# Kernel optimization log

Measured on AMD Instinct MI355X. Metric: run time of the kernel, lower is better.

## Reference

```python
import jax, jax.numpy as jnp
import numpy as np

NUM_HEADS = 8
EPS = 1e-12  # tf.nn.l2_normalize epsilon


def _l2_normalize(t):
    # tf.nn.l2_normalize: x * rsqrt(max(sum(x^2), eps)) along last axis
    sq = jnp.sum(t * t, axis=-1, keepdims=True)
    return t * jax.lax.rsqrt(jnp.maximum(sq, EPS))


def setup_inputs() -> dict:
    key = jax.random.key(0)
    ks = jax.random.split(key, 4)
    B, N, C = 8, 4096, 512
    x = jax.random.normal(ks[0], (B, N, C), dtype=jnp.float32)
    w_qkv = jax.random.normal(ks[1], (C, 3 * C), dtype=jnp.float32) * (C ** -0.5)
    b_qkv = jnp.zeros((3 * C,), dtype=jnp.float32)
    w_proj = jax.random.normal(ks[2], (C, C), dtype=jnp.float32) * (C ** -0.5)
    b_proj = jnp.zeros((C,), dtype=jnp.float32)
    return {"x": x, "w_qkv": w_qkv, "b_qkv": b_qkv, "w_proj": w_proj, "b_proj": b_proj}


def reference(x, w_qkv, b_qkv, w_proj, b_proj):
    B, N, C = x.shape
    h = NUM_HEADS
    d = C // h
    scale = d ** -0.5
    qkv = x @ w_qkv + b_qkv                        # [B,N,3C]
    qkv = qkv.reshape(B, N, 3, h, d)
    qkv = jnp.transpose(qkv, (2, 0, 3, 1, 4))      # [3,B,h,N,d]
    q, k, v = qkv[0], qkv[1], qkv[2]
    q = _l2_normalize(q) * scale
    k = _l2_normalize(k)
    # channel-wise attention: q^T k over tokens -> [B,h,d,d]
    attn = jnp.einsum('bhnd,bhne->bhde', q, k)
    attn = jax.nn.softmax(attn, axis=-1)
    out = jnp.einsum('bhnd,bhde->bhne', v, attn)   # [B,h,N,d]
    out = jnp.transpose(out, (0, 2, 1, 3)).reshape(B, N, C)
    out = out @ w_proj + b_proj
    return out
```

## Files before the change

kernel.cpp:

```cpp
#include <hip/hip_runtime.h>
#include <stdint.h>

#define NB 8
#define NN 4096
#define NC 512
#define NH 8
#define ATTN_CH 16

typedef __bf16 bf16x8 __attribute__((ext_vector_type(8)));
typedef float floatx4 __attribute__((ext_vector_type(4)));

__device__ __forceinline__ unsigned short f2bf(float f) {
  union { float f; unsigned u; } v; v.f = f;
  return (unsigned short)((v.u + 0x7fffu + ((v.u >> 16) & 1u)) >> 16);
}
__device__ __forceinline__ float2 bfp2f(unsigned u) {
  union { unsigned x; float f; } lo, hi;
  lo.x = u << 16; hi.x = u & 0xffff0000u;
  return make_float2(lo.f, hi.f);
}

__device__ __forceinline__ void async_ld16(void* lds, const void* g) {
  auto* gp = (const __attribute__((address_space(1))) unsigned int*)(uintptr_t)g;
  auto* lp = (__attribute__((address_space(3))) unsigned int*)(uintptr_t)lds;
  __builtin_amdgcn_global_load_lds(gp, lp, 16, 0, 0);
}

__global__ __launch_bounds__(256) void k_prep(const float* __restrict__ x,
                                              unsigned short* __restrict__ xb,
                                              const float* __restrict__ w,
                                              unsigned short* __restrict__ wt) {
  int bid = blockIdx.x;
  if (bid < 16384) {
    int i = (bid * 256 + threadIdx.x) * 4;
    float4 v = *(const float4*)(x + i);
    ushort4 o;
    o.x = f2bf(v.x); o.y = f2bf(v.y); o.z = f2bf(v.z); o.w = f2bf(v.w);
    *(ushort4*)(xb + i) = o;
    return;
  }
  __shared__ float tile[64][65];
  int b2 = bid - 16384;
  int nn0 = (b2 % 24) * 64, kk0 = (b2 / 24) * 64;
  int t = threadIdx.x;
#pragma unroll
  for (int i = 0; i < 16; i++) {
    int id = t + i * 256;
    int r = id >> 6, c = id & 63;
    tile[c][r] = w[(size_t)(kk0 + r) * 1536 + nn0 + c];
  }
  __syncthreads();
#pragma unroll
  for (int i = 0; i < 16; i++) {
    int id = t + i * 256;
    int rn = id >> 6, ck = id & 63;
    wt[(size_t)(nn0 + rn) * 512 + kk0 + ck] = f2bf(tile[rn][ck]);
  }
}

__global__ __launch_bounds__(256, 2) void k_gemm_qkv(const unsigned short* __restrict__ A,
                                                     const unsigned short* __restrict__ Bt,
                                                     const float* __restrict__ bias,
                                                     unsigned short* __restrict__ Cq) {
  const int LDA = 512, LDB = 512, LDC = 1536;
  int bid = blockIdx.x;
  int xcd = bid & 7, local = bid >> 3;
  int mloc = local / 12, nt = local - mloc * 12;
  int m0 = (xcd * 32 + mloc) * 128, n0 = nt * 128;

  int tid = threadIdx.x;
  int lane = tid & 63, w = tid >> 6;
  int wm = (w & 1) * 64, wn = (w >> 1) * 64;
  int quad = lane >> 4, rr = lane & 15;
  int r8 = lane >> 3, cg = lane & 7;
  int cgs8 = (cg ^ r8) * 8;
  const int swz = rr & 7;

  __shared__ __align__(16) unsigned short Als[3][128 * 64];
  __shared__ __align__(16) unsigned short Bls[2][128 * 64];

  floatx4 acc[4][4];
#pragma unroll
  for (int i = 0; i < 4; i++)
#pragma unroll
    for (int j = 0; j < 4; j++) acc[i][j] = (floatx4){0.f, 0.f, 0.f, 0.f};

  auto stageA = [&](int ss, int kt) {
    int k0 = kt << 6;
#pragma unroll
    for (int i = 0; i < 4; i++) {
      int rb = i * 32 + w * 8;
      async_ld16(&Als[ss][rb * 64], A + (size_t)(m0 + rb + r8) * LDA + k0 + cgs8);
    }
  };
  auto stageB = [&](int ss, int kt) {
    int k0 = kt << 6;
#pragma unroll
    for (int i = 0; i < 4; i++) {
      int rb = i * 32 + w * 8;
      async_ld16(&Bls[ss][rb * 64], Bt + (size_t)(n0 + rb + r8) * LDB + k0 + cgs8);
    }
  };

  auto computeK = [&](int sa, int sb, int gb) {
    bf16x8 af[4], bfr[4];
#pragma unroll
    for (int mi = 0; mi < 4; mi++)
      af[mi] = *(const bf16x8*)&Als[sa][(wm + mi * 16 + rr) * 64 + (((gb + quad) ^ swz)) * 8];
#pragma unroll
    for (int ni = 0; ni < 4; ni++)
      bfr[ni] = *(const bf16x8*)&Bls[sb][(wn + ni * 16 + rr) * 64 + (((gb + quad) ^ swz)) * 8];
    __builtin_amdgcn_s_setprio(1);
#pragma unroll
    for (int mi = 0; mi < 4; mi++)
#pragma unroll
      for (int ni = 0; ni < 4; ni++)
        acc[mi][ni] = __builtin_amdgcn_mfma_f32_16x16x32_bf16(af[mi], bfr[ni], acc[mi][ni], 0, 0, 0);
    __builtin_amdgcn_s_setprio(0);
  };

  stageB(0, 0); stageA(0, 0); stageA(1, 1);
  int sa = 0;
#pragma unroll 1
  for (int t = 0; t < 8; t++) {
    if (t < 7) asm volatile("s_waitcnt vmcnt(4)" ::: "memory");
    else       asm volatile("s_waitcnt vmcnt(0)" ::: "memory");
    asm volatile("s_barrier" ::: "memory");
    if (t < 7) stageB((t + 1) & 1, t + 1);
    if (t < 6) { int s2 = sa + 2; if (s2 >= 3) s2 -= 3; stageA(s2, t + 2); }
    __builtin_amdgcn_sched_barrier(0);
    computeK(sa, t & 1, 0);
    computeK(sa, t & 1, 4);
    sa = (sa + 1 < 3) ? sa + 1 : 0;
  }

#pragma unroll
  for (int ni = 0; ni < 4; ni++) {
    int col = n0 + wn + ni * 16 + rr;
    float bv = bias[col];
#pragma unroll
    for (int mi = 0; mi < 4; mi++) {
      int rbase = m0 + wm + mi * 16 + quad * 4;
#pragma unroll
      for (int r = 0; r < 4; r++)
        Cq[(size_t)(rbase + r) * LDC + col] = f2bf(acc[mi][ni][r] + bv);
    }
  }
}

__global__ __launch_bounds__(256) void k_attn(const unsigned short* __restrict__ QKV,
                                              float* __restrict__ logits_p) {
  int chunk = blockIdx.x, hh = blockIdx.y, b = blockIdx.z;
  int tid = threadIdx.x, w = tid >> 6, l = tid & 63;
  int quad = l >> 4, rr = l & 15;

  __shared__ __align__(16) unsigned char smem[40960];
  unsigned short* qT = (unsigned short*)smem + w * 5120;
  unsigned short* kT = qT + 2560;
  float* ps = (float*)smem;

  floatx4 acc[4][4];
#pragma unroll
  for (int i = 0; i < 4; i++)
#pragma unroll
    for (int j = 0; j < 4; j++) acc[i][j] = (floatx4){0.f, 0.f, 0.f, 0.f};

  int tok8 = l >> 3;
  int seg = l & 7;
  int sw = seg & 3;

  for (int s = 0; s < 2; s++) {
    int nbase = chunk * 256 + w * 64 + s * 32;
#pragma unroll
    for (int c = 0; c < 4; c++) {
      int n = nbase + c * 8 + tok8;
      const unsigned short* p = QKV + (size_t)(b * 4096 + n) * 1536 + hh * 64 + seg * 8;
      uint4 vq = *(const uint4*)p;
      uint4 vk = *(const uint4*)(p + 512);
      unsigned uq[4] = {vq.x, vq.y, vq.z, vq.w};
      unsigned uk[4] = {vk.x, vk.y, vk.z, vk.w};
      float qf[8], kf[8], sq = 0.f, sk = 0.f;
#pragma unroll
      for (int e = 0; e < 4; e++) {
        float2 f = bfp2f(uq[e]); qf[2 * e] = f.x; qf[2 * e + 1] = f.y; sq += f.x * f.x + f.y * f.y;
        float2 g = bfp2f(uk[e]); kf[2 * e] = g.x; kf[2 * e + 1] = g.y; sk += g.x * g.x + g.y * g.y;
      }
      sq += __shfl_xor(sq, 1); sq += __shfl_xor(sq, 2); sq += __shfl_xor(sq, 4);
      sk += __shfl_xor(sk, 1); sk += __shfl_xor(sk, 2); sk += __shfl_xor(sk, 4);
      float scq = 0.125f * rsqrtf(fmaxf(sq, 1e-12f));
      float sck = rsqrtf(fmaxf(sk, 1e-12f));
      int col = ((c ^ sw) << 3) + tok8;
#pragma unroll
      for (int j = 0; j < 8; j++) {
        int dim = seg * 8 + j;
        qT[dim * 40 + col] = f2bf(qf[j] * scq);
        kT[dim * 40 + col] = f2bf(kf[j] * sck);
      }
    }
    bf16x8 af[4], bfr[4];
#pragma unroll
    for (int mi = 0; mi < 4; mi++) {
      int s3 = (mi * 2 + (rr >> 3)) & 3;
      int off = (mi * 16 + rr) * 40 + ((quad ^ s3) << 3);
      af[mi] = *(const bf16x8*)(qT + off);
      bfr[mi] = *(const bf16x8*)(kT + off);
    }
#pragma unroll
    for (int mi = 0; mi < 4; mi++)
#pragma unroll
      for (int ni = 0; ni < 4; ni++)
        acc[mi][ni] = __builtin_amdgcn_mfma_f32_16x16x32_bf16(af[mi], bfr[ni], acc[mi][ni], 0, 0, 0);
  }

  __syncthreads();
  for (int r2 = 0; r2 < 4; r2++) {
    if (w == r2) {
#pragma unroll
      for (int mi = 0; mi < 4; mi++)
#pragma unroll
        for (int ni = 0; ni < 4; ni++)
#pragma unroll
          for (int r = 0; r < 4; r++) {
            int d = mi * 16 + quad * 4 + r, e = ni * 16 + rr;
            if (r2 == 0) ps[d * 64 + e] = acc[mi][ni][r];
            else         ps[d * 64 + e] += acc[mi][ni][r];
          }
    }
    __syncthreads();
  }
  float* outp = logits_p + ((size_t)(b * 8 + hh) * ATTN_CH + chunk) * 4096;
  for (int i = tid; i < 4096; i += 256) outp[i] = ps[i];
}

__global__ __launch_bounds__(256) void k_softmax_m(const float* __restrict__ logits_p,
                                                   const float* __restrict__ wproj,
                                                   unsigned short* __restrict__ Mt) {
  int cc = blockIdx.x & 3, rh = blockIdx.x >> 2;
  int hh = blockIdx.y, b = blockIdx.z;
  int t = threadIdx.x;
  __shared__ float ls[32][64];
  __shared__ float red[32][8];
  __shared__ float inv[32];
  const float* lp = logits_p + (size_t)((b * 8 + hh) * ATTN_CH) * 4096 + rh * 2048;
#pragma unroll
  for (int i = 0; i < 8; i++) {
    int id = t + i * 256;
    float s = 0.f;
#pragma unroll
    for (int c = 0; c < ATTN_CH; c++) s += lp[c * 4096 + id];
    ls[id >> 6][id & 63] = s;
  }
  __syncthreads();
  int row = t >> 3, part = t & 7;
  float mx = -1e30f;
#pragma unroll
  for (int j = 0; j < 8; j++) mx = fmaxf(mx, ls[row][part * 8 + j]);
  red[row][part] = mx;
  __syncthreads();
  if (part == 0) {
    float m2 = red[row][0];
#pragma unroll
    for (int j = 1; j < 8; j++) m2 = fmaxf(m2, red[row][j]);
    inv[row] = m2;
  }
  __syncthreads();
  float rm = inv[row];
  float s = 0.f;
#pragma unroll
  for (int j = 0; j < 8; j++) {
    float e = __expf(ls[row][part * 8 + j] - rm);
    ls[row][part * 8 + j] = e;
    s += e;
  }
  red[row][part] = s;
  __syncthreads();
  if (part == 0) {
    float s2 = 0.f;
#pragma unroll
    for (int j = 0; j < 8; j++) s2 += red[row][j];
    inv[row] = 1.0f / s2;
  }
  __syncthreads();

  int cout = cc * 128 + (t & 127);
  int half = t >> 7;
  float wreg[64];
#pragma unroll
  for (int ee = 0; ee < 64; ee++) wreg[ee] = wproj[(size_t)(hh * 64 + ee) * 512 + cout];
  unsigned short ob[16];
#pragma unroll
  for (int d2 = 0; d2 < 16; d2++) {
    int dd = half * 16 + d2;
    float a = 0.f;
#pragma unroll
    for (int e4 = 0; e4 < 16; e4++) {
      float4 p4 = *(const float4*)&ls[dd][e4 * 4];
      a += p4.x * wreg[e4 * 4] + p4.y * wreg[e4 * 4 + 1] + p4.z * wreg[e4 * 4 + 2] + p4.w * wreg[e4 * 4 + 3];
    }
    ob[d2] = f2bf(a * inv[dd]);
  }
  uint4* dst = (uint4*)(Mt + ((size_t)(b * 512 + cout)) * 512 + hh * 64 + rh * 32 + half * 16);
  dst[0] = ((const uint4*)ob)[0];
  dst[1] = ((const uint4*)ob)[1];
}

__global__ __launch_bounds__(256, 2) void k_gemm_out(const unsigned short* __restrict__ QKV,
                                                     const unsigned short* __restrict__ MtAll,
                                                     const float* __restrict__ bias,
                                                     float* __restrict__ Out) {
  const int LDA = 1536, LDB = 512, LDC = 512;
  int bid = blockIdx.x;
  int xcd = bid & 7, local = bid >> 3;
  int mloc = local >> 2, nt = local & 3;
  int g = xcd * 32 + mloc;
  int b = g >> 5;
  int m0 = (g & 31) * 128;
  int n0 = nt * 128;
  const unsigned short* A = QKV + (size_t)b * NN * 1536 + 1024;
  const unsigned short* Bt = MtAll + (size_t)b * 512 * 512;
  int tid = threadIdx.x;
  int lane = tid & 63, w = tid >> 6;
  int wm = (w & 1) * 64, wn = (w >> 1) * 64;
  int quad = lane >> 4, rr = lane & 15;
  int r8 = lane >> 3, cg = lane & 7;
  int cgs8 = (cg ^ r8) * 8;
  const int swz = rr & 7;

  __shared__ __align__(16) unsigned short Als[3][128 * 64];
  __shared__ __align__(16) unsigned short Bls[2][128 * 64];

  floatx4 acc[4][4];
#pragma unroll
  for (int i = 0; i < 4; i++)
#pragma unroll
    for (int j = 0; j < 4; j++) acc[i][j] = (floatx4){0.f, 0.f, 0.f, 0.f};

  auto stageA = [&](int ss, int kt) {
    int k0 = kt << 6;
#pragma unroll
    for (int i = 0; i < 4; i++) {
      int rb = i * 32 + w * 8;
      async_ld16(&Als[ss][rb * 64], A + (size_t)(m0 + rb + r8) * LDA + k0 + cgs8);
    }
  };
  auto stageB = [&](int ss, int kt) {
    int k0 = kt << 6;
#pragma unroll
    for (int i = 0; i < 4; i++) {
      int rb = i * 32 + w * 8;
      async_ld16(&Bls[ss][rb * 64], Bt + (size_t)(n0 + rb + r8) * LDB + k0 + cgs8);
    }
  };

  auto computeK = [&](int sa, int sb, int gb) {
    bf16x8 af[4], bfr[4];
#pragma unroll
    for (int mi = 0; mi < 4; mi++)
      af[mi] = *(const bf16x8*)&Als[sa][(wm + mi * 16 + rr) * 64 + (((gb + quad) ^ swz)) * 8];
#pragma unroll
    for (int ni = 0; ni < 4; ni++)
      bfr[ni] = *(const bf16x8*)&Bls[sb][(wn + ni * 16 + rr) * 64 + (((gb + quad) ^ swz)) * 8];
    __builtin_amdgcn_s_setprio(1);
#pragma unroll
    for (int mi = 0; mi < 4; mi++)
#pragma unroll
      for (int ni = 0; ni < 4; ni++)
        acc[mi][ni] = __builtin_amdgcn_mfma_f32_16x16x32_bf16(af[mi], bfr[ni], acc[mi][ni], 0, 0, 0);
    __builtin_amdgcn_s_setprio(0);
  };

  stageB(0, 0); stageA(0, 0); stageA(1, 1);
  int sa = 0;
#pragma unroll 1
  for (int t = 0; t < 8; t++) {
    if (t < 7) asm volatile("s_waitcnt vmcnt(4)" ::: "memory");
    else       asm volatile("s_waitcnt vmcnt(0)" ::: "memory");
    asm volatile("s_barrier" ::: "memory");
    if (t < 7) stageB((t + 1) & 1, t + 1);
    if (t < 6) { int s2 = sa + 2; if (s2 >= 3) s2 -= 3; stageA(s2, t + 2); }
    __builtin_amdgcn_sched_barrier(0);
    computeK(sa, t & 1, 0);
    computeK(sa, t & 1, 4);
    sa = (sa + 1 < 3) ? sa + 1 : 0;
  }

#pragma unroll
  for (int ni = 0; ni < 4; ni++) {
    int col = n0 + wn + ni * 16 + rr;
    float bv = bias[col];
#pragma unroll
    for (int mi = 0; mi < 4; mi++) {
      int rbase = m0 + wm + mi * 16 + quad * 4;
#pragma unroll
      for (int r = 0; r < 4; r++)
        Out[(size_t)b * NN * LDC + (size_t)(rbase + r) * LDC + col] = acc[mi][ni][r] + bv;
    }
  }
}

extern "C" void kernel_launch(void* const* d_in, const int* in_sizes, int n_in,
                              void* d_out, int out_size, void* d_ws, size_t ws_size,
                              hipStream_t stream) {
  const float* x      = (const float*)d_in[0];
  const float* w_qkv  = (const float*)d_in[1];
  const float* b_qkv  = (const float*)d_in[2];
  const float* w_proj = (const float*)d_in[3];
  const float* b_proj = (const float*)d_in[4];
  float* out = (float*)d_out;

  char* ws = (char*)d_ws;
  size_t off = 0;
  auto alloc = [&](size_t bytes) -> void* {
    void* p = ws + off;
    off += (bytes + 255) & ~(size_t)255;
    return p;
  };
  unsigned short* xb       = (unsigned short*)alloc((size_t)NB * NN * NC * 2);
  unsigned short* wT       = (unsigned short*)alloc((size_t)1536 * 512 * 2);
  unsigned short* qkvb     = (unsigned short*)alloc((size_t)NB * NN * 3 * NC * 2);
  float*          logits_p = (float*)alloc((size_t)NB * NH * ATTN_CH * 4096 * 4);
  unsigned short* Mt       = (unsigned short*)alloc((size_t)NB * 512 * 512 * 2);

  k_prep<<<16576, 256, 0, stream>>>(x, xb, w_qkv, wT);
  k_gemm_qkv<<<3072, 256, 0, stream>>>(xb, wT, b_qkv, qkvb);
  k_attn<<<dim3(ATTN_CH, 8, 8), 256, 0, stream>>>(qkvb, logits_p);
  k_softmax_m<<<dim3(8, 8, 8), 256, 0, stream>>>(logits_p, w_proj, Mt);
  k_gemm_out<<<1024, 256, 0, stream>>>(qkvb, Mt, b_proj, out);
}
```

Baseline: 260.4 us.

## Load GEMM B operand straight to registers and fully unroll the K loop

In both the QKV GEMM and the output-projection GEMM, the B tile no longer goes through shared memory. Each wave now loads its B fragments directly from global memory into a double-buffered register set, and the K loop is fully unrolled with a macro. The aim is to cut LDS footprint and LDS read traffic, along with the B async-copy bookkeeping. In exchange, waves that share a column tile issue duplicate, less coalesced global loads, and register pressure rises by about 64 VGPRs.

```diff
diff --git a/kernel.cpp b/kernel.cpp
--- a/kernel.cpp
+++ b/kernel.cpp
@@ -77,13 +77,14 @@
   const int swz = rr & 7;
 
   __shared__ __align__(16) unsigned short Als[3][128 * 64];
-  __shared__ __align__(16) unsigned short Bls[2][128 * 64];
 
   floatx4 acc[4][4];
 #pragma unroll
   for (int i = 0; i < 4; i++)
 #pragma unroll
     for (int j = 0; j < 4; j++) acc[i][j] = (floatx4){0.f, 0.f, 0.f, 0.f};
+
+  const unsigned short* Bbase = Bt + (size_t)(n0 + wn + rr) * LDB + quad * 8;
 
   auto stageA = [&](int ss, int kt) {
     int k0 = kt << 6;
@@ -93,46 +94,45 @@
       async_ld16(&Als[ss][rb * 64], A + (size_t)(m0 + rb + r8) * LDA + k0 + cgs8);
     }
   };
-  auto stageB = [&](int ss, int kt) {
+  auto loadB = [&](int kt, bf16x8 (&dst)[4][2]) {
     int k0 = kt << 6;
 #pragma unroll
-    for (int i = 0; i < 4; i++) {
-      int rb = i * 32 + w * 8;
-      async_ld16(&Bls[ss][rb * 64], Bt + (size_t)(n0 + rb + r8) * LDB + k0 + cgs8);
-    }
-  };
-
-  auto computeK = [&](int sa, int sb, int gb) {
-    bf16x8 af[4], bfr[4];
+    for (int ni = 0; ni < 4; ni++)
+#pragma unroll
+      for (int g = 0; g < 2; g++)
+        dst[ni][g] = *(const bf16x8*)(Bbase + (size_t)(ni * 16) * LDB + k0 + g * 32);
+  };
+  auto computeK = [&](int sa, bf16x8 (&bfr)[4][2], int g) {
+    bf16x8 af[4];
 #pragma unroll
     for (int mi = 0; mi < 4; mi++)
-      af[mi] = *(const bf16x8*)&Als[sa][(wm + mi * 16 + rr) * 64 + (((gb + quad) ^ swz)) * 8];
-#pragma unroll
-    for (int ni = 0; ni < 4; ni++)
-      bfr[ni] = *(const bf16x8*)&Bls[sb][(wn + ni * 16 + rr) * 64 + (((gb + quad) ^ swz)) * 8];
+      af[mi] = *(const bf16x8*)&Als[sa][(wm + mi * 16 + rr) * 64 + (((g * 4 + quad) ^ swz)) * 8];
     __builtin_amdgcn_s_setprio(1);
 #pragma unroll
     for (int mi = 0; mi < 4; mi++)
 #pragma unroll
       for (int ni = 0; ni < 4; ni++)
-        acc[mi][ni] = __builtin_amdgcn_mfma_f32_16x16x32_bf16(af[mi], bfr[ni], acc[mi][ni], 0, 0, 0);
+        acc[mi][ni] = __builtin_amdgcn_mfma_f32_16x16x32_bf16(af[mi], bfr[ni][g], acc[mi][ni], 0, 0, 0);
     __builtin_amdgcn_s_setprio(0);
   };
 
-  stageB(0, 0); stageA(0, 0); stageA(1, 1);
-  int sa = 0;
-#pragma unroll 1
-  for (int t = 0; t < 8; t++) {
-    if (t < 7) asm volatile("s_waitcnt vmcnt(4)" ::: "memory");
-    else       asm volatile("s_waitcnt vmcnt(0)" ::: "memory");
-    asm volatile("s_barrier" ::: "memory");
-    if (t < 7) stageB((t + 1) & 1, t + 1);
-    if (t < 6) { int s2 = sa + 2; if (s2 >= 3) s2 -= 3; stageA(s2, t + 2); }
-    __builtin_amdgcn_sched_barrier(0);
-    computeK(sa, t & 1, 0);
-    computeK(sa, t & 1, 4);
-    sa = (sa + 1 < 3) ? sa + 1 : 0;
-  }
+#define GSTEP(k, bc, bn)                                              \
+  {                                                                   \
+    if ((k) < 7) asm volatile("s_waitcnt vmcnt(4)" ::: "memory");     \
+    else         asm volatile("s_waitcnt vmcnt(0)" ::: "memory");     \
+    asm volatile("s_barrier" ::: "memory");                           \
+    if ((k) < 7) loadB((k) + 1, bn);                                  \
+    if ((k) < 6) stageA(((k) + 2) % 3, (k) + 2);                      \
+    __builtin_amdgcn_sched_barrier(0);                                \
+    computeK((k) % 3, bc, 0);                                         \
+    computeK((k) % 3, bc, 1);                                         \
+  }
+
+  bf16x8 bX[4][2], bY[4][2];
+  stageA(0, 0); loadB(0, bX); stageA(1, 1);
+  GSTEP(0, bX, bY); GSTEP(1, bY, bX); GSTEP(2, bX, bY); GSTEP(3, bY, bX);
+  GSTEP(4, bX, bY); GSTEP(5, bY, bX); GSTEP(6, bX, bY); GSTEP(7, bY, bX);
+#undef GSTEP
 
 #pragma unroll
   for (int ni = 0; ni < 4; ni++) {
@@ -312,9 +312,9 @@
   int bid = blockIdx.x;
   int xcd = bid & 7, local = bid >> 3;
   int mloc = local >> 2, nt = local & 3;
-  int g = xcd * 32 + mloc;
-  int b = g >> 5;
-  int m0 = (g & 31) * 128;
+  int g2 = xcd * 32 + mloc;
+  int b = g2 >> 5;
+  int m0 = (g2 & 31) * 128;
   int n0 = nt * 128;
   const unsigned short* A = QKV + (size_t)b * NN * 1536 + 1024;
   const unsigned short* Bt = MtAll + (size_t)b * 512 * 512;
@@ -327,13 +327,14 @@
   const int swz = rr & 7;
 
   __shared__ __align__(16) unsigned short Als[3][128 * 64];
-  __shared__ __align__(16) unsigned short Bls[2][128 * 64];
 
   floatx4 acc[4][4];
 #pragma unroll
   for (int i = 0; i < 4; i++)
 #pragma unroll
     for (int j = 0; j < 4; j++) acc[i][j] = (floatx4){0.f, 0.f, 0.f, 0.f};
+
+  const unsigned short* Bbase = Bt + (size_t)(n0 + wn + rr) * LDB + quad * 8;
 
   auto stageA = [&](int ss, int kt) {
     int k0 = kt << 6;
@@ -343,46 +344,45 @@
       async_ld16(&Als[ss][rb * 64], A + (size_t)(m0 + rb + r8) * LDA + k0 + cgs8);
     }
   };
-  auto stageB = [&](int ss, int kt) {
+  auto loadB = [&](int kt, bf16x8 (&dst)[4][2]) {
     int k0 = kt << 6;
 #pragma unroll
-    for (int i = 0; i < 4; i++) {
-      int rb = i * 32 + w * 8;
-      async_ld16(&Bls[ss][rb * 64], Bt + (size_t)(n0 + rb + r8) * LDB + k0 + cgs8);
-    }
-  };
-
-  auto computeK = [&](int sa, int sb, int gb) {
-    bf16x8 af[4], bfr[4];
+    for (int ni = 0; ni < 4; ni++)
+#pragma unroll
+      for (int g = 0; g < 2; g++)
+        dst[ni][g] = *(const bf16x8*)(Bbase + (size_t)(ni * 16) * LDB + k0 + g * 32);
+  };
+  auto computeK = [&](int sa, bf16x8 (&bfr)[4][2], int g) {
+    bf16x8 af[4];
 #pragma unroll
     for (int mi = 0; mi < 4; mi++)
-      af[mi] = *(const bf16x8*)&Als[sa][(wm + mi * 16 + rr) * 64 + (((gb + quad) ^ swz)) * 8];
-#pragma unroll
-    for (int ni = 0; ni < 4; ni++)
-      bfr[ni] = *(const bf16x8*)&Bls[sb][(wn + ni * 16 + rr) * 64 + (((gb + quad) ^ swz)) * 8];
+      af[mi] = *(const bf16x8*)&Als[sa][(wm + mi * 16 + rr) * 64 + (((g * 4 + quad) ^ swz)) * 8];
     __builtin_amdgcn_s_setprio(1);
 #pragma unroll
     for (int mi = 0; mi < 4; mi++)
 #pragma unroll
       for (int ni = 0; ni < 4; ni++)
-        acc[mi][ni] = __builtin_amdgcn_mfma_f32_16x16x32_bf16(af[mi], bfr[ni], acc[mi][ni], 0, 0, 0);
+        acc[mi][ni] = __builtin_amdgcn_mfma_f32_16x16x32_bf16(af[mi], bfr[ni][g], acc[mi][ni], 0, 0, 0);
     __builtin_amdgcn_s_setprio(0);
   };
 
-  stageB(0, 0); stageA(0, 0); stageA(1, 1);
-  int sa = 0;
-#pragma unroll 1
-  for (int t = 0; t < 8; t++) {
-    if (t < 7) asm volatile("s_waitcnt vmcnt(4)" ::: "memory");
-    else       asm volatile("s_waitcnt vmcnt(0)" ::: "memory");
-    asm volatile("s_barrier" ::: "memory");
-    if (t < 7) stageB((t + 1) & 1, t + 1);
-    if (t < 6) { int s2 = sa + 2; if (s2 >= 3) s2 -= 3; stageA(s2, t + 2); }
-    __builtin_amdgcn_sched_barrier(0);
-    computeK(sa, t & 1, 0);
-    computeK(sa, t & 1, 4);
-    sa = (sa + 1 < 3) ? sa + 1 : 0;
-  }
+#define GSTEP(k, bc, bn)                                              \
+  {                                                                   \
+    if ((k) < 7) asm volatile("s_waitcnt vmcnt(4)" ::: "memory");     \
+    else         asm volatile("s_waitcnt vmcnt(0)" ::: "memory");     \
+    asm volatile("s_barrier" ::: "memory");                           \
+    if ((k) < 7) loadB((k) + 1, bn);                                  \
+    if ((k) < 6) stageA(((k) + 2) % 3, (k) + 2);                      \
+    __builtin_amdgcn_sched_barrier(0);                                \
+    computeK((k) % 3, bc, 0);                                         \
+    computeK((k) % 3, bc, 1);                                         \
+  }
+
+  bf16x8 bX[4][2], bY[4][2];
+  stageA(0, 0); loadB(0, bX); stageA(1, 1);
+  GSTEP(0, bX, bY); GSTEP(1, bY, bX); GSTEP(2, bX, bY); GSTEP(3, bY, bX);
+  GSTEP(4, bX, bY); GSTEP(5, bY, bX); GSTEP(6, bX, bY); GSTEP(7, bY, bX);
+#undef GSTEP
 
 #pragma unroll
   for (int ni = 0; ni < 4; ni++) {
```

Measured after the change: 321.3 us. +23.4%, slower.
